# Performance work log

Hardware: AMD Instinct MI355X
Metric: run time of the kernel (lower is better)

Reference implementation:

```python
import jax, jax.numpy as jnp
import numpy as np

TEMPERATURE = 0.5
EPS = 1e-8
NEG = -1e30  # effectively -inf for masked logits


def _l2norm(x):
    n = jnp.sqrt(jnp.sum(x * x, axis=1, keepdims=True))
    return x / jnp.maximum(n, EPS)


def setup_inputs() -> dict:
    key = jax.random.key(0)
    ks = jax.random.split(key, 4)
    N, D = 2048, 128
    return {f"projection_image_aug{i+1}": jax.random.normal(ks[i], (N, D), dtype=jnp.float32)
            for i in range(4)}


def reference(projection_image_aug1, projection_image_aug2,
              projection_image_aug3, projection_image_aug4):
    zs = [projection_image_aug1.astype(jnp.float32),
          projection_image_aug2.astype(jnp.float32),
          projection_image_aug3.astype(jnp.float32),
          projection_image_aug4.astype(jnp.float32)]
    N = zs[0].shape[0]
    k = len(zs)
    z = jnp.concatenate(zs[:2], axis=0)        # [2N, D]
    z_all = jnp.concatenate(zs, axis=0)        # [kN, D]
    # cosine sim via normalize + matmul (same math as broadcast CosineSimilarity)
    sim = _l2norm(z) @ _l2norm(z_all).T / TEMPERATURE   # [2N, kN]

    rows = jnp.arange(2 * N)
    half = rows // N                 # 0 for first N rows, 1 for second
    idx = rows % N
    cols = jnp.arange(k * N)
    block = cols // N
    # mask: diagonal entries of every N-block except the target block (1-half)
    diag = (cols[None, :] % N) == idx[:, None]
    mask = diag & (block[None, :] != (1 - half)[:, None])
    sim_m = jnp.where(mask, NEG, sim)
    # positive column: aug2 partner for rows<N, aug1 partner for rows>=N
    target_col = (1 - half) * N + idx
    pos = jnp.take_along_axis(sim_m, target_col[:, None], axis=1)[:, 0]
    # cross_entropy(reduction='sum') / (2N)
    loss = jnp.sum(jax.nn.logsumexp(sim_m, axis=1) - pos) / (2 * N)
    return loss
```

## Files before the change

kernel.cpp:

```cpp
#include <hip/hip_runtime.h>
#include <hip/hip_bf16.h>


#define NN      2048
#define DD      128
#define TWO_N   4096
#define FOUR_N  8192
#define BM      128
#define BN      128
#define GT      8
#define CTG     8

using frag_ab = __attribute__((ext_vector_type(8))) short;
using f32x4   = __attribute__((ext_vector_type(4))) float;

__device__ inline void gl_lds16(const short* g, short* l) {
  __builtin_amdgcn_global_load_lds(
      (const __attribute__((address_space(1))) void*)g,
      (__attribute__((address_space(3))) void*)l, 16, 0, 0);
}

__device__ inline int swz(int chunk) {
  return (chunk & ~15) | ((chunk & 15) ^ ((chunk >> 4) & 15));
}

__global__ __launch_bounds__(256) void knorm(const float* __restrict__ p0,
                                             const float* __restrict__ p1,
                                             const float* __restrict__ p2,
                                             const float* __restrict__ p3,
                                             short* __restrict__ Bn,
                                             float* __restrict__ out) {
  if (blockIdx.x == 0 && threadIdx.x == 0) out[0] = 0.0f;
  int wave = threadIdx.x >> 6, lane = threadIdx.x & 63;
  int row = blockIdx.x * 4 + wave;
  int q = row >> 11, idx = row & (NN - 1);
  const float* src = (q == 0) ? p0 : (q == 1) ? p1 : (q == 2) ? p2 : p3;
  const float2* s2 = (const float2*)(src + (size_t)idx * DD);
  float2 v = s2[lane];
  float ss = v.x * v.x + v.y * v.y;
  #pragma unroll
  for (int sh = 1; sh < 64; sh <<= 1) ss += __shfl_xor(ss, sh, 64);
  float inv = 1.0f / fmaxf(sqrtf(ss), 1e-8f);
  __hip_bfloat162 o;
  o.x = __float2bfloat16(v.x * inv);
  o.y = __float2bfloat16(v.y * inv);
  ((__hip_bfloat162*)(Bn + (size_t)row * DD))[lane] = o;
}

__global__ __launch_bounds__(512, 1) void kgemm(const short* __restrict__ Bn,
                                                float* __restrict__ pS) {
  __shared__ short sA[BM * DD];
  __shared__ short sB[2][BN * DD];
  __shared__ float sS[BM][4];

  int t = threadIdx.x, wave = t >> 6, lane = t & 63;
  int quad = lane >> 4, l16 = lane & 15;
  int rowHalf = wave >> 2, colQ = wave & 3;

  const short* gA = Bn + (size_t)blockIdx.x * BM * DD;
  const short* gB0 = Bn + (size_t)blockIdx.y * (GT * BN) * DD;

  #pragma unroll
  for (int i = 0; i < 4; ++i) {
    int c0 = i * 512 + wave * 64;
    gl_lds16(gA + (size_t)swz(c0 + lane) * 8, sA + (size_t)c0 * 8);
    gl_lds16(gB0 + (size_t)swz(c0 + lane) * 8, sB[0] + (size_t)c0 * 8);
  }
  __syncthreads();

  frag_ab a[4][4];
  #pragma unroll
  for (int k = 0; k < 4; ++k)
    #pragma unroll
    for (int rf = 0; rf < 4; ++rf) {
      int r_ = rowHalf * 64 + rf * 16 + l16;
      a[k][rf] = *(const frag_ab*)&sA[(size_t)((r_ << 4) | ((k * 4 + quad) ^ l16)) * 8];
    }

  float sAcc[4][4];
  #pragma unroll
  for (int rf = 0; rf < 4; ++rf)
    #pragma unroll
    for (int r = 0; r < 4; ++r) sAcc[rf][r] = 0.f;

  #pragma unroll 1
  for (int g = 0; g < GT; ++g) {
    if (g < GT - 1) {
      const short* gBn = gB0 + (size_t)(g + 1) * BN * DD;
      short* dst = sB[(g + 1) & 1];
      #pragma unroll
      for (int i = 0; i < 4; ++i) {
        int c0 = i * 512 + wave * 64;
        gl_lds16(gBn + (size_t)swz(c0 + lane) * 8, dst + (size_t)c0 * 8);
      }
    }
    const short* sBg = sB[g & 1];

    f32x4 acc[4][2];
    #pragma unroll
    for (int rf = 0; rf < 4; ++rf)
      #pragma unroll
      for (int cf = 0; cf < 2; ++cf) acc[rf][cf] = (f32x4){0.f, 0.f, 0.f, 0.f};

    #pragma unroll
    for (int k = 0; k < 4; ++k) {
      frag_ab b[2];
      #pragma unroll
      for (int cf = 0; cf < 2; ++cf) {
        int r_ = colQ * 32 + cf * 16 + l16;
        b[cf] = *(const frag_ab*)&sBg[(size_t)((r_ << 4) | ((k * 4 + quad) ^ l16)) * 8];
      }
      #pragma unroll
      for (int rf = 0; rf < 4; ++rf)
        #pragma unroll
        for (int cf = 0; cf < 2; ++cf)
          acc[rf][cf] = __builtin_amdgcn_mfma_f32_16x16x32_bf16(a[k][rf], b[cf], acc[rf][cf], 0, 0, 0);
    }

    #pragma unroll
    for (int rf = 0; rf < 4; ++rf)
      #pragma unroll
      for (int r = 0; r < 4; ++r) {
        #pragma unroll
        for (int cf = 0; cf < 2; ++cf)
          sAcc[rf][r] += __expf(fmaf(acc[rf][cf][r], 2.0f, -2.0f));
      }
    __syncthreads();
  }

  #pragma unroll
  for (int rf = 0; rf < 4; ++rf)
    #pragma unroll
    for (int r = 0; r < 4; ++r) {
      float s = sAcc[rf][r];
      #pragma unroll
      for (int sh = 1; sh < 16; sh <<= 1) s += __shfl_xor(s, sh, 64);
      if (l16 == 0) sS[rowHalf * 64 + rf * 16 + quad * 4 + r][colQ] = s;
    }
  __syncthreads();
  if (t < BM)
    pS[(size_t)(blockIdx.x * BM + t) * CTG + blockIdx.y] =
        (sS[t][0] + sS[t][1]) + (sS[t][2] + sS[t][3]);
}

__global__ __launch_bounds__(256) void kfin(const short* __restrict__ Bn,
                                            const float* __restrict__ pS,
                                            float* __restrict__ out) {
  int t = threadIdx.x, wave = t >> 6, lane = t & 63;
  int grBase = blockIdx.x * BM;
  __shared__ float sRed[4];

  float wloss = 0.f;
  for (int rr = wave; rr < BM; rr += 4) {
    int gr = grBase + rr;
    int idx = gr & (NN - 1), half = gr >> 11;
    float S = (lane < CTG) ? pS[(size_t)gr * CTG + lane] : 0.f;
    #pragma unroll
    for (int sh = 1; sh < 8; sh <<= 1) S += __shfl_xor(S, sh, 64);
    unsigned int ua = ((const unsigned int*)(Bn + (size_t)gr * DD))[lane];
    unsigned int ub = ((const unsigned int*)(Bn + (size_t)((1 - half) * NN + idx) * DD))[lane];
    unsigned int uc = ((const unsigned int*)(Bn + (size_t)(2 * NN + idx) * DD))[lane];
    unsigned int ud = ((const unsigned int*)(Bn + (size_t)(3 * NN + idx) * DD))[lane];
    float a0 = __uint_as_float((ua & 0xffffu) << 16), a1 = __uint_as_float(ua & 0xffff0000u);
    float b0 = __uint_as_float((ub & 0xffffu) << 16), b1 = __uint_as_float(ub & 0xffff0000u);
    float c0 = __uint_as_float((uc & 0xffffu) << 16), c1 = __uint_as_float(uc & 0xffff0000u);
    float d0 = __uint_as_float((ud & 0xffffu) << 16), d1 = __uint_as_float(ud & 0xffff0000u);
    float daa = a0 * a0 + a1 * a1;
    float dab = a0 * b0 + a1 * b1;
    float dac = a0 * c0 + a1 * c1;
    float dad = a0 * d0 + a1 * d1;
    #pragma unroll
    for (int sh = 1; sh < 64; sh <<= 1) {
      daa += __shfl_xor(daa, sh, 64);
      dab += __shfl_xor(dab, sh, 64);
      dac += __shfl_xor(dac, sh, 64);
      dad += __shfl_xor(dad, sh, 64);
    }
    float Sc = S - __expf(fmaf(daa, 2.0f, -2.0f))
                 - __expf(fmaf(dac, 2.0f, -2.0f))
                 - __expf(fmaf(dad, 2.0f, -2.0f));
    float loss = (2.0f + __logf(Sc)) - 2.0f * dab;
    if (lane == 0) wloss += loss;
  }
  if (lane == 0) sRed[wave] = wloss;
  __syncthreads();
  if (t == 0)
    atomicAdd(out, (sRed[0] + sRed[1] + sRed[2] + sRed[3]) * (1.0f / (float)TWO_N));
}

extern "C" void kernel_launch(void* const* d_in, const int* in_sizes, int n_in,
                              void* d_out, int out_size, void* d_ws, size_t ws_size,
                              hipStream_t stream) {
  (void)in_sizes; (void)n_in; (void)out_size; (void)ws_size;
  const float* p0 = (const float*)d_in[0];
  const float* p1 = (const float*)d_in[1];
  const float* p2 = (const float*)d_in[2];
  const float* p3 = (const float*)d_in[3];

  short* Bn = (short*)d_ws;
  float* pS = (float*)((char*)d_ws + (size_t)FOUR_N * DD * sizeof(short));
  float* out = (float*)d_out;

  knorm<<<FOUR_N / 4, 256, 0, stream>>>(p0, p1, p2, p3, Bn, out);
  kgemm<<<dim3(TWO_N / BM, CTG), 512, 0, stream>>>(Bn, pS);
  kfin<<<TWO_N / BM, 256, 0, stream>>>(Bn, pS, out);
}
```

Before: 105.6 us.

## Load B fragments directly from global into registers, drop LDS B buffers

The GEMM kernel no longer stages B tiles through double-buffered LDS with async global-to-LDS loads. Each wave now loads its B MFMA fragments straight from global memory into registers, prefetching the next tile while computing the current one. This removes the per-iteration __syncthreads and cuts LDS use, and launch bounds are raised to allow two blocks per CU. In exchange, B rows shared across waves are loaded redundantly from global/L2 with less coalescing, and register pressure rises.

After: 109.4 us. +3.6%, slower.

```diff
diff --git a/kernel.cpp b/kernel.cpp
--- a/kernel.cpp
+++ b/kernel.cpp
@@ -47,10 +47,9 @@
   ((__hip_bfloat162*)(Bn + (size_t)row * DD))[lane] = o;
 }
 
-__global__ __launch_bounds__(512, 1) void kgemm(const short* __restrict__ Bn,
+__global__ __launch_bounds__(512, 2) void kgemm(const short* __restrict__ Bn,
                                                 float* __restrict__ pS) {
   __shared__ short sA[BM * DD];
-  __shared__ short sB[2][BN * DD];
   __shared__ float sS[BM][4];
 
   int t = threadIdx.x, wave = t >> 6, lane = t & 63;
@@ -58,13 +57,10 @@
   int rowHalf = wave >> 2, colQ = wave & 3;
 
   const short* gA = Bn + (size_t)blockIdx.x * BM * DD;
-  const short* gB0 = Bn + (size_t)blockIdx.y * (GT * BN) * DD;
-
   #pragma unroll
   for (int i = 0; i < 4; ++i) {
     int c0 = i * 512 + wave * 64;
     gl_lds16(gA + (size_t)swz(c0 + lane) * 8, sA + (size_t)c0 * 8);
-    gl_lds16(gB0 + (size_t)swz(c0 + lane) * 8, sB[0] + (size_t)c0 * 8);
   }
   __syncthreads();
 
@@ -77,6 +73,15 @@
       a[k][rf] = *(const frag_ab*)&sA[(size_t)((r_ << 4) | ((k * 4 + quad) ^ l16)) * 8];
     }
 
+  const short* gB = Bn + (size_t)(blockIdx.y * (GT * BN) + colQ * 32 + l16) * DD + quad * 8;
+
+  frag_ab bc[8], bn_[8];
+  #pragma unroll
+  for (int cf = 0; cf < 2; ++cf)
+    #pragma unroll
+    for (int k = 0; k < 4; ++k)
+      bc[cf * 4 + k] = *(const frag_ab*)(gB + (size_t)cf * 16 * DD + k * 32);
+
   float sAcc[4][4];
   #pragma unroll
   for (int rf = 0; rf < 4; ++rf)
@@ -85,16 +90,14 @@
 
   #pragma unroll 1
   for (int g = 0; g < GT; ++g) {
-    if (g < GT - 1) {
-      const short* gBn = gB0 + (size_t)(g + 1) * BN * DD;
-      short* dst = sB[(g + 1) & 1];
-      #pragma unroll
-      for (int i = 0; i < 4; ++i) {
-        int c0 = i * 512 + wave * 64;
-        gl_lds16(gBn + (size_t)swz(c0 + lane) * 8, dst + (size_t)c0 * 8);
-      }
-    }
-    const short* sBg = sB[g & 1];
+    if (g + 1 < GT) {
+      const short* gB2 = gB + (size_t)(g + 1) * BN * DD;
+      #pragma unroll
+      for (int cf = 0; cf < 2; ++cf)
+        #pragma unroll
+        for (int k = 0; k < 4; ++k)
+          bn_[cf * 4 + k] = *(const frag_ab*)(gB2 + (size_t)cf * 16 * DD + k * 32);
+    }
 
     f32x4 acc[4][2];
     #pragma unroll
@@ -103,19 +106,12 @@
       for (int cf = 0; cf < 2; ++cf) acc[rf][cf] = (f32x4){0.f, 0.f, 0.f, 0.f};
 
     #pragma unroll
-    for (int k = 0; k < 4; ++k) {
-      frag_ab b[2];
-      #pragma unroll
-      for (int cf = 0; cf < 2; ++cf) {
-        int r_ = colQ * 32 + cf * 16 + l16;
-        b[cf] = *(const frag_ab*)&sBg[(size_t)((r_ << 4) | ((k * 4 + quad) ^ l16)) * 8];
-      }
+    for (int k = 0; k < 4; ++k)
       #pragma unroll
       for (int rf = 0; rf < 4; ++rf)
         #pragma unroll
         for (int cf = 0; cf < 2; ++cf)
-          acc[rf][cf] = __builtin_amdgcn_mfma_f32_16x16x32_bf16(a[k][rf], b[cf], acc[rf][cf], 0, 0, 0);
-    }
+          acc[rf][cf] = __builtin_amdgcn_mfma_f32_16x16x32_bf16(a[k][rf], bc[cf * 4 + k], acc[rf][cf], 0, 0, 0);
 
     #pragma unroll
     for (int rf = 0; rf < 4; ++rf)
@@ -125,7 +121,9 @@
         for (int cf = 0; cf < 2; ++cf)
           sAcc[rf][r] += __expf(fmaf(acc[rf][cf][r], 2.0f, -2.0f));
       }
-    __syncthreads();
+
+    #pragma unroll
+    for (int i = 0; i < 8; ++i) bc[i] = bn_[i];
   }
 
   #pragma unroll
```
